# Optimization experiments

Measured on AMD Instinct MI355X. Metric: run time of the kernel, lower is better.

Reference implementation:

```python
import jax, jax.numpy as jnp
import numpy as np

IN_DIM, H, D = 45, 128, 256

def setup_inputs() -> dict:
    key = jax.random.key(0)
    ks = jax.random.split(key, 9)
    s_in = 1.0 / np.sqrt(IN_DIM)
    s_h = 1.0 / np.sqrt(H)
    return {
        "pose": jax.random.normal(ks[0], (64, 4096, 9, 5), dtype=jnp.float32),
        "ln1_g": jnp.ones((IN_DIM,), jnp.float32),
        "ln1_b": jnp.zeros((IN_DIM,), jnp.float32),
        "w1": jax.random.uniform(ks[1], (IN_DIM, H), jnp.float32, -s_in, s_in),
        "b1": jax.random.uniform(ks[2], (H,), jnp.float32, -s_in, s_in),
        "w2": jax.random.uniform(ks[3], (H, D), jnp.float32, -s_h, s_h),
        "b2": jax.random.uniform(ks[4], (D,), jnp.float32, -s_h, s_h),
        "ln2_g": jnp.ones((D,), jnp.float32),
        "ln2_b": jnp.zeros((D,), jnp.float32),
    }

def _layernorm(x, g, b, eps=1e-5):
    mu = jnp.mean(x, axis=-1, keepdims=True)
    var = jnp.mean(jnp.square(x - mu), axis=-1, keepdims=True)
    return (x - mu) * jax.lax.rsqrt(var + eps) * g + b

def reference(pose, ln1_g, ln1_b, w1, b1, w2, b2, ln2_g, ln2_b):
    B, T, J, C = pose.shape
    x = pose.reshape(B, T, J * C)                      # [B,T,45]
    x = _layernorm(x, ln1_g, ln1_b)
    x = jnp.einsum('btf,fh->bth', x, w1) + b1          # [B,T,128]
    x = jax.nn.gelu(x, approximate=False)              # torch GELU default = exact erf
    # dropout is identity in eval mode
    x = jnp.einsum('bth,hd->btd', x, w2) + b2          # [B,T,256]
    return _layernorm(x, ln2_g, ln2_b)
```

## Files before the change

kernel.cpp:

```cpp
#include <hip/hip_runtime.h>
#include <cstdint>

#define IN_DIM 45
#define HDIM 128
#define DDIM 256
#define ROWS 64
#define NBLK 4096

typedef unsigned short u16;
typedef __attribute__((ext_vector_type(8))) short v8s;
typedef __attribute__((ext_vector_type(4))) float f32x4;

__device__ __forceinline__ u16 f2bf(float x){
  uint32_t u = __float_as_uint(x);
  u += 0x7FFFu + ((u >> 16) & 1u);
  return (u16)(u >> 16);
}

__device__ __forceinline__ void g2l16(const void* g, void* l){
  __builtin_amdgcn_global_load_lds(
      (const __attribute__((address_space(1))) unsigned int*)g,
      (__attribute__((address_space(3))) unsigned int*)l, 16, 0, 0);
}

__global__ void prep_kernel(const float* __restrict__ w1, const float* __restrict__ w2,
                            u16* __restrict__ w1s, u16* __restrict__ w2s){
  int idx = blockIdx.x*256 + threadIdx.x;
  if (idx < 128*64){
    int n = idx >> 6, k = idx & 63;
    int gp = (k >> 3) ^ (n & 7);
    float v = (k < IN_DIM) ? w1[k*HDIM + n] : 0.f;
    w1s[(n << 6) | (gp << 3) | (k & 7)] = f2bf(v);
  } else if (idx < 128*64 + 256*128){
    int t = idx - 128*64;
    int n = t >> 7, k = t & 127;
    int gp = ((k >> 3) ^ (n & 15));
    w2s[(n << 7) | (gp << 3) | (k & 7)] = f2bf(w2[k*DDIM + n]);
  }
}

__global__ __launch_bounds__(256, 2)
void posemlp_kernel(const float* __restrict__ pose,
                    const float* __restrict__ ln1g, const float* __restrict__ ln1b,
                    const float* __restrict__ b1v,  const float* __restrict__ b2v,
                    const float* __restrict__ ln2g, const float* __restrict__ ln2b,
                    const u16* __restrict__ w1s, const u16* __restrict__ w2s,
                    float* __restrict__ out)
{
  __shared__ __align__(16) unsigned char smem[43008];
  u16*  sw = (u16*)smem;
  u16*  sx = (u16*)(smem + 16384);
  u16*  sh = (u16*)(smem + 25600);
  float* posel = (float*)(smem + 25600);

  const int tid = threadIdx.x;
  const int blk = blockIdx.x;

  {
    const char* psrc = (const char*)pose + (size_t)blk * (ROWS*IN_DIM*4);
    #pragma unroll
    for (int j = 0; j < 3; ++j){
      int i = j*256 + tid;
      if (i < 720) g2l16(psrc + (size_t)i*16, smem + 25600 + i*16);
    }
    const char* wsrc = (const char*)w1s;
    #pragma unroll
    for (int j = 0; j < 4; ++j){
      int i = j*256 + tid;
      g2l16(wsrc + (size_t)i*16, smem + i*16);
    }
  }
  __syncthreads();

  {
    int row = tid >> 2, p = tid & 3;
    const float* pr = posel + row*IN_DIM;
    float sum = 0.f, sq = 0.f;
    for (int k = p; k < IN_DIM; k += 4){ float v = pr[k]; sum += v; sq += v*v; }
    sum += __shfl_xor(sum, 1); sum += __shfl_xor(sum, 2);
    sq  += __shfl_xor(sq, 1);  sq  += __shfl_xor(sq, 2);
    float mu = sum * (1.f/IN_DIM);
    float rs = rsqrtf(sq * (1.f/IN_DIM) - mu*mu + 1e-5f);
    u16* xr = sx + row*72;
    for (int k = p; k < IN_DIM; k += 4){
      float v = (pr[k] - mu) * rs * ln1g[k] + ln1b[k];
      xr[k] = f2bf(v);
    }
    for (int k = IN_DIM + p; k < 64; k += 4) xr[k] = 0;
  }
  __syncthreads();

  const int lane = tid & 63, wv = tid >> 6;
  const int col = lane & 15, quad = lane >> 4;

  f32x4 acc1[8];
  #pragma unroll
  for (int i = 0; i < 8; ++i) acc1[i] = (f32x4){0.f,0.f,0.f,0.f};
  {
    const u16* xa = sx + (16*wv + col)*72;
    #pragma unroll
    for (int ks = 0; ks < 2; ++ks){
      v8s a = *(const v8s*)(xa + ks*32 + quad*8);
      #pragma unroll
      for (int nt = 0; nt < 8; ++nt){
        int n = nt*16 + col;
        int gp = (ks*4 + quad) ^ (n & 7);
        v8s b = *(const v8s*)(sw + n*64 + gp*8);
        acc1[nt] = __builtin_amdgcn_mfma_f32_16x16x32_bf16(a, b, acc1[nt], 0, 0, 0);
      }
    }
  }
  #pragma unroll
  for (int nt = 0; nt < 8; ++nt){
    int n = nt*16 + col;
    float bias = b1v[n];
    #pragma unroll
    for (int r = 0; r < 4; ++r){
      float v = acc1[nt][r] + bias;
      v = 0.5f * v * (1.f + erff(v * 0.70710678118654752f));
      sh[(16*wv + quad*4 + r)*136 + n] = f2bf(v);
    }
  }
  __syncthreads();

  v8s a2[4];
  {
    const u16* ha = sh + (16*wv + col)*136;
    #pragma unroll
    for (int ks = 0; ks < 4; ++ks) a2[ks] = *(const v8s*)(ha + ks*32 + quad*8);
  }

  f32x4 acc2[16];
  #pragma unroll
  for (int i = 0; i < 16; ++i) acc2[i] = (f32x4){0.f,0.f,0.f,0.f};
  const char* w2b = (const char*)w2s;
  #pragma unroll
  for (int hq = 0; hq < 4; ++hq){
    #pragma unroll
    for (int j = 0; j < 4; ++j){
      int i = j*256 + tid;
      g2l16(w2b + (size_t)hq*16384 + (size_t)i*16, smem + i*16);
    }
    __syncthreads();
    #pragma unroll
    for (int ntl = 0; ntl < 4; ++ntl){
      int nq = ntl*16 + col;
      #pragma unroll
      for (int ks = 0; ks < 4; ++ks){
        int gp = (ks*4 + quad) ^ (nq & 15);
        v8s b = *(const v8s*)(sw + nq*128 + gp*8);
        acc2[hq*4 + ntl] = __builtin_amdgcn_mfma_f32_16x16x32_bf16(a2[ks], b, acc2[hq*4 + ntl], 0, 0, 0);
      }
    }
    __syncthreads();
  }

  float sum[4] = {0,0,0,0}, sq[4] = {0,0,0,0};
  #pragma unroll
  for (int i = 0; i < 16; ++i){
    float bb = b2v[i*16 + col];
    #pragma unroll
    for (int r = 0; r < 4; ++r){
      float v = acc2[i][r] + bb;
      acc2[i][r] = v;
      sum[r] += v; sq[r] += v*v;
    }
  }
  #pragma unroll
  for (int m = 1; m <= 8; m <<= 1){
    #pragma unroll
    for (int r = 0; r < 4; ++r){
      sum[r] += __shfl_xor(sum[r], m);
      sq[r]  += __shfl_xor(sq[r], m);
    }
  }
  float mu[4], rs[4];
  #pragma unroll
  for (int r = 0; r < 4; ++r){
    mu[r] = sum[r] * (1.f/DDIM);
    rs[r] = rsqrtf(sq[r] * (1.f/DDIM) - mu[r]*mu[r] + 1e-5f);
  }
  const int rbase = blk*ROWS + 16*wv + quad*4;
  #pragma unroll
  for (int r = 0; r < 4; ++r){
    #pragma unroll
    for (int i = 0; i < 16; ++i){
      int n = i*16 + col;
      out[(size_t)(rbase + r)*DDIM + n] =
          (acc2[i][r] - mu[r]) * rs[r] * ln2g[n] + ln2b[n];
    }
  }
}

extern "C" void kernel_launch(void* const* d_in, const int* in_sizes, int n_in,
                              void* d_out, int out_size, void* d_ws, size_t ws_size,
                              hipStream_t stream){
  const float* pose = (const float*)d_in[0];
  const float* ln1g = (const float*)d_in[1];
  const float* ln1b = (const float*)d_in[2];
  const float* w1   = (const float*)d_in[3];
  const float* b1   = (const float*)d_in[4];
  const float* w2   = (const float*)d_in[5];
  const float* b2   = (const float*)d_in[6];
  const float* ln2g = (const float*)d_in[7];
  const float* ln2b = (const float*)d_in[8];
  u16* w1s = (u16*)d_ws;
  u16* w2s = (u16*)((char*)d_ws + 16384);
  prep_kernel<<<160, 256, 0, stream>>>(w1, w2, w1s, w2s);
  posemlp_kernel<<<NBLK, 256, 0, stream>>>(pose, ln1g, ln1b, b1, b2, ln2g, ln2b,
                                           w1s, w2s, (float*)d_out);
}
```

Before: 394.4 us.

## Keep weights in registers and loop persistent blocks over double-buffered row tiles

```diff
diff --git a/kernel.cpp b/kernel.cpp
--- a/kernel.cpp
+++ b/kernel.cpp
@@ -5,11 +5,13 @@
 #define HDIM 128
 #define DDIM 256
 #define ROWS 64
-#define NBLK 4096
+#define NT 8
+#define NBLK 512
 
 typedef unsigned short u16;
 typedef __attribute__((ext_vector_type(8))) short v8s;
 typedef __attribute__((ext_vector_type(4))) float f32x4;
+typedef __attribute__((ext_vector_type(2))) float f32x2;
 
 __device__ __forceinline__ u16 f2bf(float x){
   uint32_t u = __float_as_uint(x);
@@ -24,18 +26,22 @@
 }
 
 __global__ void prep_kernel(const float* __restrict__ w1, const float* __restrict__ w2,
-                            u16* __restrict__ w1s, u16* __restrict__ w2s){
+                            u16* __restrict__ w1f, u16* __restrict__ w2f){
   int idx = blockIdx.x*256 + threadIdx.x;
-  if (idx < 128*64){
-    int n = idx >> 6, k = idx & 63;
-    int gp = (k >> 3) ^ (n & 7);
+  if (idx < 8192){
+    int j = idx & 7, lane = (idx >> 3) & 63, f = idx >> 9;
+    int wv = f >> 2, ks = (f >> 1) & 1, nt = f & 1;
+    int n = wv*32 + nt*16 + (lane & 15);
+    int k = ks*32 + (lane >> 4)*8 + j;
     float v = (k < IN_DIM) ? w1[k*HDIM + n] : 0.f;
-    w1s[(n << 6) | (gp << 3) | (k & 7)] = f2bf(v);
-  } else if (idx < 128*64 + 256*128){
-    int t = idx - 128*64;
-    int n = t >> 7, k = t & 127;
-    int gp = ((k >> 3) ^ (n & 15));
-    w2s[(n << 7) | (gp << 3) | (k & 7)] = f2bf(w2[k*DDIM + n]);
+    w1f[idx] = f2bf(v);
+  } else if (idx < 40960){
+    int t = idx - 8192;
+    int j = t & 7, lane = (t >> 3) & 63, f = t >> 9;
+    int wv = f >> 4, ks = (f >> 2) & 3, ntl = f & 3;
+    int n = wv*64 + ntl*16 + (lane & 15);
+    int k = ks*32 + (lane >> 4)*8 + j;
+    w2f[t] = f2bf(w2[k*DDIM + n]);
   }
 }
 
@@ -44,150 +50,186 @@
                     const float* __restrict__ ln1g, const float* __restrict__ ln1b,
                     const float* __restrict__ b1v,  const float* __restrict__ b2v,
                     const float* __restrict__ ln2g, const float* __restrict__ ln2b,
-                    const u16* __restrict__ w1s, const u16* __restrict__ w2s,
+                    const u16* __restrict__ w1f, const u16* __restrict__ w2f,
                     float* __restrict__ out)
 {
-  __shared__ __align__(16) unsigned char smem[43008];
-  u16*  sw = (u16*)smem;
-  u16*  sx = (u16*)(smem + 16384);
-  u16*  sh = (u16*)(smem + 25600);
-  float* posel = (float*)(smem + 25600);
-
-  const int tid = threadIdx.x;
-  const int blk = blockIdx.x;
-
+  __shared__ __align__(16) unsigned char smem[51712];
+  u16*   sx    = (u16*)(smem + 23040);
+  u16*   sh    = (u16*)(smem + 32256);
+  f32x2* stats = (f32x2*)(smem + 49664);
+
+  const int tid  = threadIdx.x;
+  const int lane = tid & 63, wv = tid >> 6;
+  const int col  = lane & 15, quad = lane >> 4;
+
+  v8s b1f[2][2], b2f[4][4];
   {
-    const char* psrc = (const char*)pose + (size_t)blk * (ROWS*IN_DIM*4);
+    const v8s* p1 = (const v8s*)w1f;
+    #pragma unroll
+    for (int ks = 0; ks < 2; ++ks)
+      #pragma unroll
+      for (int nt = 0; nt < 2; ++nt)
+        b1f[ks][nt] = p1[((wv*2 + ks)*2 + nt)*64 + lane];
+    const v8s* p2 = (const v8s*)w2f;
+    #pragma unroll
+    for (int ks = 0; ks < 4; ++ks)
+      #pragma unroll
+      for (int ntl = 0; ntl < 4; ++ntl)
+        b2f[ks][ntl] = p2[((wv*4 + ks)*4 + ntl)*64 + lane];
+  }
+  float bias1[2], bias2[4], g2[4], bt2[4];
+  #pragma unroll
+  for (int nt = 0; nt < 2; ++nt) bias1[nt] = b1v[wv*32 + nt*16 + col];
+  #pragma unroll
+  for (int ntl = 0; ntl < 4; ++ntl){
+    int n = wv*64 + ntl*16 + col;
+    bias2[ntl] = b2v[n]; g2[ntl] = ln2g[n]; bt2[ntl] = ln2b[n];
+  }
+
+  {
+    f32x4* z = (f32x4*)sx;
+    for (int i = tid; i < 576; i += 256) z[i] = (f32x4){0.f,0.f,0.f,0.f};
+  }
+  const size_t tile0 = (size_t)blockIdx.x * NT;
+  {
+    const char* psrc = (const char*)pose + tile0 * (ROWS*IN_DIM*4);
     #pragma unroll
     for (int j = 0; j < 3; ++j){
       int i = j*256 + tid;
-      if (i < 720) g2l16(psrc + (size_t)i*16, smem + 25600 + i*16);
-    }
-    const char* wsrc = (const char*)w1s;
-    #pragma unroll
-    for (int j = 0; j < 4; ++j){
-      int i = j*256 + tid;
-      g2l16(wsrc + (size_t)i*16, smem + i*16);
+      if (i < 720) g2l16(psrc + (size_t)i*16, smem + i*16);
     }
   }
   __syncthreads();
 
-  {
-    int row = tid >> 2, p = tid & 3;
-    const float* pr = posel + row*IN_DIM;
-    float sum = 0.f, sq = 0.f;
-    for (int k = p; k < IN_DIM; k += 4){ float v = pr[k]; sum += v; sq += v*v; }
-    sum += __shfl_xor(sum, 1); sum += __shfl_xor(sum, 2);
-    sq  += __shfl_xor(sq, 1);  sq  += __shfl_xor(sq, 2);
-    float mu = sum * (1.f/IN_DIM);
-    float rs = rsqrtf(sq * (1.f/IN_DIM) - mu*mu + 1e-5f);
-    u16* xr = sx + row*72;
-    for (int k = p; k < IN_DIM; k += 4){
-      float v = (pr[k] - mu) * rs * ln1g[k] + ln1b[k];
-      xr[k] = f2bf(v);
-    }
-    for (int k = IN_DIM + p; k < 64; k += 4) xr[k] = 0;
-  }
-  __syncthreads();
-
-  const int lane = tid & 63, wv = tid >> 6;
-  const int col = lane & 15, quad = lane >> 4;
-
-  f32x4 acc1[8];
-  #pragma unroll
-  for (int i = 0; i < 8; ++i) acc1[i] = (f32x4){0.f,0.f,0.f,0.f};
-  {
-    const u16* xa = sx + (16*wv + col)*72;
+  #pragma unroll 1
+  for (int t = 0; t < NT; ++t){
+    const int cur = t & 1;
+    const float* posel = (const float*)(smem + cur*11520);
+
+    {
+      int row = tid >> 2, p = tid & 3;
+      const float* pr = posel + row*IN_DIM;
+      float sum = 0.f, sq = 0.f;
+      for (int k = p; k < IN_DIM; k += 4){ float v = pr[k]; sum += v; sq += v*v; }
+      sum += __shfl_xor(sum, 1); sum += __shfl_xor(sum, 2);
+      sq  += __shfl_xor(sq, 1);  sq  += __shfl_xor(sq, 2);
+      float mu = sum * (1.f/IN_DIM);
+      float rs = rsqrtf(sq * (1.f/IN_DIM) - mu*mu + 1e-5f);
+      u16* xr = sx + row*72;
+      for (int k = p; k < IN_DIM; k += 4)
+        xr[k] = f2bf((pr[k] - mu) * rs * ln1g[k] + ln1b[k]);
+    }
+    __syncthreads();
+
+    if (t + 1 < NT){
+      const char* psrc = (const char*)pose + (tile0 + t + 1) * (ROWS*IN_DIM*4);
+      unsigned char* pdst = smem + (cur^1)*11520;
+      #pragma unroll
+      for (int j = 0; j < 3; ++j){
+        int i = j*256 + tid;
+        if (i < 720) g2l16(psrc + (size_t)i*16, pdst + (size_t)i*16);
+      }
+    }
+
+    f32x4 acc1[4][2];
+    #pragma unroll
+    for (int mt = 0; mt < 4; ++mt)
+      #pragma unroll
+      for (int nt = 0; nt < 2; ++nt) acc1[mt][nt] = (f32x4){0.f,0.f,0.f,0.f};
     #pragma unroll
     for (int ks = 0; ks < 2; ++ks){
-      v8s a = *(const v8s*)(xa + ks*32 + quad*8);
-      #pragma unroll
-      for (int nt = 0; nt < 8; ++nt){
-        int n = nt*16 + col;
-        int gp = (ks*4 + quad) ^ (n & 7);
-        v8s b = *(const v8s*)(sw + n*64 + gp*8);
-        acc1[nt] = __builtin_amdgcn_mfma_f32_16x16x32_bf16(a, b, acc1[nt], 0, 0, 0);
+      v8s a[4];
+      #pragma unroll
+      for (int mt = 0; mt < 4; ++mt)
+        a[mt] = *(const v8s*)(sx + (mt*16 + col)*72 + ks*32 + quad*8);
+      #pragma unroll
+      for (int mt = 0; mt < 4; ++mt)
+        #pragma unroll
+        for (int nt = 0; nt < 2; ++nt)
+          acc1[mt][nt] = __builtin_amdgcn_mfma_f32_16x16x32_bf16(a[mt], b1f[ks][nt], acc1[mt][nt], 0, 0, 0);
+    }
+    #pragma unroll
+    for (int mt = 0; mt < 4; ++mt)
+      #pragma unroll
+      for (int nt = 0; nt < 2; ++nt){
+        #pragma unroll
+        for (int r = 0; r < 4; ++r){
+          float v = acc1[mt][nt][r] + bias1[nt];
+          v = 0.5f * v * (1.f + erff(v * 0.70710678118654752f));
+          sh[(mt*16 + quad*4 + r)*136 + wv*32 + nt*16 + col] = f2bf(v);
+        }
       }
-    }
-  }
-  #pragma unroll
-  for (int nt = 0; nt < 8; ++nt){
-    int n = nt*16 + col;
-    float bias = b1v[n];
-    #pragma unroll
-    for (int r = 0; r < 4; ++r){
-      float v = acc1[nt][r] + bias;
-      v = 0.5f * v * (1.f + erff(v * 0.70710678118654752f));
-      sh[(16*wv + quad*4 + r)*136 + n] = f2bf(v);
-    }
-  }
-  __syncthreads();
-
-  v8s a2[4];
-  {
-    const u16* ha = sh + (16*wv + col)*136;
-    #pragma unroll
-    for (int ks = 0; ks < 4; ++ks) a2[ks] = *(const v8s*)(ha + ks*32 + quad*8);
-  }
-
-  f32x4 acc2[16];
-  #pragma unroll
-  for (int i = 0; i < 16; ++i) acc2[i] = (f32x4){0.f,0.f,0.f,0.f};
-  const char* w2b = (const char*)w2s;
-  #pragma unroll
-  for (int hq = 0; hq < 4; ++hq){
-    #pragma unroll
-    for (int j = 0; j < 4; ++j){
-      int i = j*256 + tid;
-      g2l16(w2b + (size_t)hq*16384 + (size_t)i*16, smem + i*16);
-    }
     __syncthreads();
-    #pragma unroll
-    for (int ntl = 0; ntl < 4; ++ntl){
-      int nq = ntl*16 + col;
-      #pragma unroll
-      for (int ks = 0; ks < 4; ++ks){
-        int gp = (ks*4 + quad) ^ (nq & 15);
-        v8s b = *(const v8s*)(sw + nq*128 + gp*8);
-        acc2[hq*4 + ntl] = __builtin_amdgcn_mfma_f32_16x16x32_bf16(a2[ks], b, acc2[hq*4 + ntl], 0, 0, 0);
+
+    f32x4 acc2[4][4];
+    #pragma unroll
+    for (int mt = 0; mt < 4; ++mt)
+      #pragma unroll
+      for (int ntl = 0; ntl < 4; ++ntl) acc2[mt][ntl] = (f32x4){0.f,0.f,0.f,0.f};
+    #pragma unroll
+    for (int ks = 0; ks < 4; ++ks){
+      v8s a[4];
+      #pragma unroll
+      for (int mt = 0; mt < 4; ++mt)
+        a[mt] = *(const v8s*)(sh + (mt*16 + col)*136 + ks*32 + quad*8);
+      #pragma unroll
+      for (int mt = 0; mt < 4; ++mt)
+        #pragma unroll
+        for (int ntl = 0; ntl < 4; ++ntl)
+          acc2[mt][ntl] = __builtin_amdgcn_mfma_f32_16x16x32_bf16(a[mt], b2f[ks][ntl], acc2[mt][ntl], 0, 0, 0);
+    }
+
+    float psum[4][4], psq[4][4];
+    #pragma unroll
+    for (int mt = 0; mt < 4; ++mt)
+      #pragma unroll
+      for (int r = 0; r < 4; ++r){ psum[mt][r] = 0.f; psq[mt][r] = 0.f; }
+    #pragma unroll
+    for (int mt = 0; mt < 4; ++mt)
+      #pragma unroll
+      for (int ntl = 0; ntl < 4; ++ntl)
+        #pragma unroll
+        for (int r = 0; r < 4; ++r){
+          float v = acc2[mt][ntl][r] + bias2[ntl];
+          acc2[mt][ntl][r] = v;
+          psum[mt][r] += v; psq[mt][r] += v*v;
+        }
+    #pragma unroll
+    for (int m = 1; m <= 8; m <<= 1){
+      #pragma unroll
+      for (int mt = 0; mt < 4; ++mt)
+        #pragma unroll
+        for (int r = 0; r < 4; ++r){
+          psum[mt][r] += __shfl_xor(psum[mt][r], m);
+          psq[mt][r]  += __shfl_xor(psq[mt][r],  m);
+        }
+    }
+    if (col == 0){
+      #pragma unroll
+      for (int mt = 0; mt < 4; ++mt)
+        #pragma unroll
+        for (int r = 0; r < 4; ++r)
+          stats[(mt*16 + quad*4 + r)*4 + wv] = (f32x2){psum[mt][r], psq[mt][r]};
+    }
+    __syncthreads();
+
+    const size_t rowG0 = (tile0 + t) * ROWS;
+    #pragma unroll
+    for (int mt = 0; mt < 4; ++mt){
+      #pragma unroll
+      for (int r = 0; r < 4; ++r){
+        int rowL = mt*16 + quad*4 + r;
+        f32x4 s0 = *(const f32x4*)&stats[rowL*4];
+        f32x4 s1 = *(const f32x4*)&stats[rowL*4 + 2];
+        float sum = s0.x + s0.z + s1.x + s1.z;
+        float sq  = s0.y + s0.w + s1.y + s1.w;
+        float mu = sum * (1.f/DDIM);
+        float rs = rsqrtf(sq * (1.f/DDIM) - mu*mu + 1e-5f);
+        float* orow = out + (rowG0 + rowL)*DDIM;
+        #pragma unroll
+        for (int ntl = 0; ntl < 4; ++ntl)
+          orow[wv*64 + ntl*16 + col] = (acc2[mt][ntl][r] - mu) * rs * g2[ntl] + bt2[ntl];
       }
-    }
-    __syncthreads();
-  }
-
-  float sum[4] = {0,0,0,0}, sq[4] = {0,0,0,0};
-  #pragma unroll
-  for (int i = 0; i < 16; ++i){
-    float bb = b2v[i*16 + col];
-    #pragma unroll
-    for (int r = 0; r < 4; ++r){
-      float v = acc2[i][r] + bb;
-      acc2[i][r] = v;
-      sum[r] += v; sq[r] += v*v;
-    }
-  }
-  #pragma unroll
-  for (int m = 1; m <= 8; m <<= 1){
-    #pragma unroll
-    for (int r = 0; r < 4; ++r){
-      sum[r] += __shfl_xor(sum[r], m);
-      sq[r]  += __shfl_xor(sq[r], m);
-    }
-  }
-  float mu[4], rs[4];
-  #pragma unroll
-  for (int r = 0; r < 4; ++r){
-    mu[r] = sum[r] * (1.f/DDIM);
-    rs[r] = rsqrtf(sq[r] * (1.f/DDIM) - mu[r]*mu[r] + 1e-5f);
-  }
-  const int rbase = blk*ROWS + 16*wv + quad*4;
-  #pragma unroll
-  for (int r = 0; r < 4; ++r){
-    #pragma unroll
-    for (int i = 0; i < 16; ++i){
-      int n = i*16 + col;
-      out[(size_t)(rbase + r)*DDIM + n] =
-          (acc2[i][r] - mu[r]) * rs[r] * ln2g[n] + ln2b[n];
     }
   }
 }
@@ -204,9 +246,9 @@
   const float* b2   = (const float*)d_in[6];
   const float* ln2g = (const float*)d_in[7];
   const float* ln2b = (const float*)d_in[8];
-  u16* w1s = (u16*)d_ws;
-  u16* w2s = (u16*)((char*)d_ws + 16384);
-  prep_kernel<<<160, 256, 0, stream>>>(w1, w2, w1s, w2s);
+  u16* w1f = (u16*)d_ws;
+  u16* w2f = (u16*)((char*)d_ws + 16384);
+  prep_kernel<<<160, 256, 0, stream>>>(w1, w2, w1f, w2f);
   posemlp_kernel<<<NBLK, 256, 0, stream>>>(pose, ln1g, ln1b, b1, b2, ln2g, ln2b,
-                                           w1s, w2s, (float*)d_out);
-}
+                                           w1f, w2f, (float*)d_out);
+}
```

Result: slower. 490.9 us (+24.5%).
